# Kernel optimization log

Hardware: AMD Instinct MI355X
Metric: run time of the kernel (lower is better)

The kernel has to match this reference:

```python
import jax, jax.numpy as jnp
import numpy as np

RES = 32            # input grid resolution
OUT_RES = 64        # after subdivide
C = 128             # channels (== out_channels -> skip is identity)
G = 32              # group-norm groups
N = 8192            # active input voxels
EPS = 1e-5

# 8 child offsets for subdivide, 27 stencil offsets for 3x3x3 submanifold conv
_OFFS8 = np.stack(np.meshgrid([0, 1], [0, 1], [0, 1], indexing='ij'), -1).reshape(-1, 3).astype(np.int32)
_OFFS27 = np.stack(np.meshgrid([-1, 0, 1], [-1, 0, 1], [-1, 0, 1], indexing='ij'), -1).reshape(-1, 3).astype(np.int32)


def group_norm(x, gamma, beta, num_groups=G, eps=EPS):
    # sparse group norm over all active voxels of the (single) sample
    n, c = x.shape
    xg = x.reshape(n, num_groups, c // num_groups)
    mean = xg.mean(axis=(0, 2), keepdims=True)
    var = xg.var(axis=(0, 2), keepdims=True)
    xn = (xg - mean) * jax.lax.rsqrt(var + eps)
    return xn.reshape(n, c) * gamma + beta


def subdivide_coords(coords):
    offs = jnp.asarray(_OFFS8)
    return (coords[:, None, :] * 2 + offs[None, :, :]).reshape(-1, 3)  # [8N, 3]


def subm_conv3d(feats, coords, W, b, grid_res):
    # submanifold 3x3x3 sparse conv: outputs only at active sites
    n = feats.shape[0]
    grid = jnp.full((grid_res, grid_res, grid_res), -1, dtype=jnp.int32)
    grid = grid.at[coords[:, 0], coords[:, 1], coords[:, 2]].set(
        jnp.arange(n, dtype=jnp.int32))
    out = jnp.zeros((n, W.shape[-1]), dtype=feats.dtype)
    for k in range(27):  # fixed small stencil loop
        off = jnp.asarray(_OFFS27[k])
        nb = coords + off
        inb = jnp.all((nb >= 0) & (nb < grid_res), axis=1)
        nbc = jnp.clip(nb, 0, grid_res - 1)
        idx = grid[nbc[:, 0], nbc[:, 1], nbc[:, 2]]
        mask = inb & (idx >= 0)
        g = jnp.where(mask[:, None], feats[jnp.where(mask, idx, 0)], 0.0)
        out = out + g @ W[k]
    return out + b


def setup_inputs() -> dict:
    key = jax.random.key(0)
    ks = jax.random.split(key, 8)
    rng = np.random.default_rng(0)
    flat = rng.choice(RES ** 3, size=N, replace=False)
    coords = np.stack([flat // (RES * RES), (flat // RES) % RES, flat % RES],
                      axis=-1).astype(np.int32)
    feats = jax.random.normal(ks[0], (N, C), dtype=jnp.float32)
    gamma1 = 1.0 + 0.1 * jax.random.normal(ks[1], (C,), dtype=jnp.float32)
    beta1 = 0.1 * jax.random.normal(ks[2], (C,), dtype=jnp.float32)
    W1 = jax.random.normal(ks[3], (27, C, C), dtype=jnp.float32) * 0.05
    b1 = jax.random.normal(ks[4], (C,), dtype=jnp.float32) * 0.05
    gamma2 = 1.0 + 0.1 * jax.random.normal(ks[5], (C,), dtype=jnp.float32)
    beta2 = 0.1 * jax.random.normal(ks[6], (C,), dtype=jnp.float32)
    W2 = jax.random.normal(ks[7], (27, C, C), dtype=jnp.float32) * 0.05
    b2 = jax.random.normal(jax.random.fold_in(key, 99), (C,), dtype=jnp.float32) * 0.05
    return {"feats": feats, "gamma1": gamma1, "beta1": beta1, "W1": W1,
            "b1": b1, "gamma2": gamma2, "beta2": beta2, "W2": W2, "b2": b2,
            "coords": jnp.asarray(coords)}


def reference(feats, gamma1, beta1, W1, b1, gamma2, beta2, W2, b2, coords):
    # act_layers: GroupNorm + SiLU at input resolution
    h = jax.nn.silu(group_norm(feats, gamma1, beta1))
    # subdivide both branch and residual (8 children per voxel)
    new_coords = subdivide_coords(coords)          # [8N, 3] in OUT_RES grid
    h = jnp.repeat(h, 8, axis=0)
    x_sub = jnp.repeat(feats, 8, axis=0)
    # out_layers: conv3 -> GN -> SiLU -> conv3 (submanifold, same active set)
    h = subm_conv3d(h, new_coords, W1, b1, OUT_RES)
    h = jax.nn.silu(group_norm(h, gamma2, beta2))
    h = subm_conv3d(h, new_coords, W2, b2, OUT_RES)
    # skip_connection is Identity since out_channels == channels
    return h + x_sub
```

## Files before the change

### kernel.cpp

```cpp
#include <hip/hip_runtime.h>

#define NPAR   8192
#define NCH    65536
#define RES    32
#define EPS    1e-5f

typedef __attribute__((ext_vector_type(8))) short short8;
typedef __attribute__((ext_vector_type(4))) float floatx4;

__device__ __forceinline__ unsigned short f2bf(float f) {
    union { float f; unsigned u; } v; v.f = f;
    unsigned r = v.u + 0x7fffu + ((v.u >> 16) & 1u);
    return (unsigned short)(r >> 16);
}
__device__ __forceinline__ float bf2f(unsigned short b) {
    union { unsigned u; float f; } v; v.u = ((unsigned)b) << 16;
    return v.f;
}
__device__ __forceinline__ void glds16(const void* g, void* l) {
    __builtin_amdgcn_global_load_lds(
        (__attribute__((address_space(1))) const void*)g,
        (__attribute__((address_space(3))) void*)l, 16, 0, 0);
}
__device__ __forceinline__ int k27_of(int o, int s) {
    return (((o >> 2) & 1) + ((s >> 2) & 1)) * 9 +
           (((o >> 1) & 1) + ((s >> 1) & 1)) * 3 +
           ((o & 1) + (s & 1));
}
__device__ __forceinline__ void axis_dlist(int o, int s, int* d, int& n) {
    if (o == 0) { if (s == 0) { d[0] = -1; n = 1; } else { d[0] = 0; d[1] = 1; n = 2; } }
    else        { if (s == 0) { d[0] = -1; d[1] = 0; n = 2; } else { d[0] = 1; n = 1; } }
}

__global__ void k1_kernel(const int* __restrict__ coords, int* __restrict__ grid32,
                          const float* __restrict__ x, float* __restrict__ sum,
                          float* __restrict__ sq,
                          const float* __restrict__ W1, const float* __restrict__ W2,
                          unsigned short* __restrict__ Wc1f, unsigned short* __restrict__ Wp2) {
    int b = blockIdx.x;
    int t = threadIdx.x;
    if (b < 32) {
        int p = b * 256 + t;
        grid32[(coords[p*3] << 10) + (coords[p*3+1] << 5) + coords[p*3+2]] = p;
    } else if (b < 248) {
        int rem = (b - 32) * 256 + t;
        int lane = rem & 63;
        int ks   = (rem >> 6) & 3;
        int nb   = (rem >> 8) & 7;
        int tap  = rem >> 11;
        int n  = nb * 16 + (lane & 15);
        int k0 = ks * 32 + (lane >> 4) * 8;
        unsigned short v[8];
#pragma unroll
        for (int j = 0; j < 8; ++j) v[j] = f2bf(W2[tap * 16384 + (k0 + j) * 128 + n]);
        uint4 pk;
        pk.x = (unsigned)v[0] | ((unsigned)v[1] << 16);
        pk.y = (unsigned)v[2] | ((unsigned)v[3] << 16);
        pk.z = (unsigned)v[4] | ((unsigned)v[5] << 16);
        pk.w = (unsigned)v[6] | ((unsigned)v[7] << 16);
        *(uint4*)&Wp2[(long)rem * 8] = pk;
    } else if (b < 760) {
        int rem = (b - 248) * 256 + t;
        int lane  = rem & 63;
        int ks    = (rem >> 6) & 3;
        int nb    = (rem >> 8) & 7;
        int combo = rem >> 11;
        int o = combo >> 3, s = combo & 7;
        int n  = nb * 16 + (lane & 15);
        int k0 = ks * 32 + (lane >> 4) * 8;
        int d0[2], d1[2], d2[2], n0, n1, n2;
        axis_dlist((o >> 2) & 1, (s >> 2) & 1, d0, n0);
        axis_dlist((o >> 1) & 1, (s >> 1) & 1, d1, n1);
        axis_dlist(o & 1,        s & 1,        d2, n2);
        unsigned short v[8];
#pragma unroll
        for (int j = 0; j < 8; ++j) {
            float acc = 0.0f;
            for (int a = 0; a < n0; ++a)
                for (int bb = 0; bb < n1; ++bb)
                    for (int cc = 0; cc < n2; ++cc) {
                        int kk = (d0[a] + 1) * 9 + (d1[bb] + 1) * 3 + (d2[cc] + 1);
                        acc += W1[kk * 16384 + (k0 + j) * 128 + n];
                    }
            v[j] = f2bf(acc);
        }
        uint4 pk;
        pk.x = (unsigned)v[0] | ((unsigned)v[1] << 16);
        pk.y = (unsigned)v[2] | ((unsigned)v[3] << 16);
        pk.z = (unsigned)v[4] | ((unsigned)v[5] << 16);
        pk.w = (unsigned)v[6] | ((unsigned)v[7] << 16);
        *(uint4*)&Wc1f[(long)rem * 8] = pk;
    } else {
        __shared__ float s_sum[32], s_sq[32];
        if (t < 32) { s_sum[t] = 0.0f; s_sq[t] = 0.0f; }
        __syncthreads();
        const float4* x4 = (const float4*)x;
        int total = NPAR * 32;
        int idx0 = (b - 760) * 256 + t;
        int g = idx0 & 31;
        float ls = 0.0f, lq = 0.0f;
        for (int idx = idx0; idx < total; idx += 256 * 256) {
            float4 v = x4[idx];
            ls += v.x + v.y + v.z + v.w;
            lq += v.x * v.x + v.y * v.y + v.z * v.z + v.w * v.w;
        }
        atomicAdd(&s_sum[g], ls);
        atomicAdd(&s_sq[g], lq);
        __syncthreads();
        if (t < 32) { atomicAdd(&sum[t], s_sum[t]); atomicAdd(&sq[t], s_sq[t]); }
    }
}

__global__ void k2_kernel(const int* __restrict__ coords, const int* __restrict__ grid32,
                          int* __restrict__ idx_tab, int* __restrict__ pidx27,
                          const float* __restrict__ x, const float* __restrict__ sum,
                          const float* __restrict__ sq, const float* __restrict__ gamma,
                          const float* __restrict__ beta, unsigned short* __restrict__ y) {
    int b = blockIdx.x;
    if (b < 32) {
        int p = b * 256 + threadIdx.x;
        int cx = coords[p*3], cy = coords[p*3+1], cz = coords[p*3+2];
        int r27[27];
#pragma unroll
        for (int k = 0; k < 27; ++k) {
            int nx = cx + k / 9 - 1, ny = cy + (k / 3) % 3 - 1, nz = cz + k % 3 - 1;
            int r = -1;
            if ((unsigned)nx < 32u && (unsigned)ny < 32u && (unsigned)nz < 32u) {
                int g = grid32[(nx << 10) + (ny << 5) + nz];
                if ((unsigned)g < (unsigned)NPAR) r = g;
            }
            r27[k] = r;
            pidx27[k * NPAR + p] = r;
        }
#pragma unroll
        for (int k = 0; k < 27; ++k) {
            const int dx = k / 9 - 1, dy = (k / 3) % 3 - 1, dz = k % 3 - 1;
            int v[8];
#pragma unroll
            for (int o = 0; o < 8; ++o) {
                const int ex = ((o >> 2) & 1) + dx;
                const int ey = ((o >> 1) & 1) + dy;
                const int ez = (o & 1) + dz;
                const int ptap = ((ex >> 1) + 1) * 9 + ((ey >> 1) + 1) * 3 + ((ez >> 1) + 1);
                const int slot = ((ex & 1) << 2) + ((ey & 1) << 1) + (ez & 1);
                int r = r27[ptap];
                v[o] = (r >= 0) ? slot * NPAR + r : -1;
            }
            int4* dst = (int4*)&idx_tab[k * NCH + p * 8];
            dst[0] = make_int4(v[0], v[1], v[2], v[3]);
            dst[1] = make_int4(v[4], v[5], v[6], v[7]);
        }
    } else {
        const float4* x4 = (const float4*)x;
        uint2* y2 = (uint2*)y;
        const float4* g4 = (const float4*)gamma;
        const float4* b4 = (const float4*)beta;
        float cnt = (float)NPAR * 4.0f;
        int total = NPAR * 32;
        for (int idx = (b - 32) * 256 + threadIdx.x; idx < total; idx += 256 * 256) {
            int c4 = idx & 31;
            float mean = sum[c4] / cnt;
            float var = sq[c4] / cnt - mean * mean;
            float rstd = rsqrtf(var + EPS);
            float4 v = x4[idx];
            float4 gm = g4[c4];
            float4 bt = b4[c4];
            float a[4] = {v.x, v.y, v.z, v.w};
            float gg[4] = {gm.x, gm.y, gm.z, gm.w};
            float bb[4] = {bt.x, bt.y, bt.z, bt.w};
            unsigned short o[4];
#pragma unroll
            for (int i = 0; i < 4; ++i) {
                float tv = (a[i] - mean) * rstd * gg[i] + bb[i];
                o[i] = f2bf(tv / (1.0f + __expf(-tv)));
            }
            uint2 pk;
            pk.x = (unsigned)o[0] | ((unsigned)o[1] << 16);
            pk.y = (unsigned)o[2] | ((unsigned)o[3] << 16);
            y2[idx] = pk;
        }
    }
}

__global__ void gn_apply_bf16_kernel(unsigned short* __restrict__ x,
                                     const float* __restrict__ sum, const float* __restrict__ sq,
                                     const float* __restrict__ gamma, const float* __restrict__ beta,
                                     int nrows) {
    uint2* x2 = (uint2*)x;
    const float4* g4 = (const float4*)gamma;
    const float4* b4 = (const float4*)beta;
    float cnt = (float)nrows * 4.0f;
    int total = nrows * 32;
    for (int idx = blockIdx.x * blockDim.x + threadIdx.x; idx < total;
         idx += gridDim.x * blockDim.x) {
        int c4 = idx & 31;
        float mean = sum[c4] / cnt;
        float var = sq[c4] / cnt - mean * mean;
        float rstd = rsqrtf(var + EPS);
        uint2 pk = x2[idx];
        float a[4] = {bf2f((unsigned short)(pk.x & 0xffff)), bf2f((unsigned short)(pk.x >> 16)),
                      bf2f((unsigned short)(pk.y & 0xffff)), bf2f((unsigned short)(pk.y >> 16))};
        float4 gm = g4[c4];
        float4 bt = b4[c4];
        float gg[4] = {gm.x, gm.y, gm.z, gm.w};
        float bb[4] = {bt.x, bt.y, bt.z, bt.w};
        unsigned short o[4];
#pragma unroll
        for (int i = 0; i < 4; ++i) {
            float tv = (a[i] - mean) * rstd * gg[i] + bb[i];
            o[i] = f2bf(tv / (1.0f + __expf(-tv)));
        }
        pk.x = (unsigned)o[0] | ((unsigned)o[1] << 16);
        pk.y = (unsigned)o[2] | ((unsigned)o[3] << 16);
        x2[idx] = pk;
    }
}

__device__ __forceinline__ void mfma_phase(
    const unsigned short* __restrict__ Abuf, short8 (&bfr)[2][4],
    floatx4 (&acc)[8][2], int aswz) {
#pragma unroll
    for (int ks = 0; ks < 4; ++ks) {
        short8 afr[8];
#pragma unroll
        for (int mt = 0; mt < 8; ++mt)
            afr[mt] = *(const short8*)&Abuf[(mt << 11) + (ks << 9) + aswz];
#pragma unroll
        for (int mt = 0; mt < 8; ++mt)
#pragma unroll
            for (int nt = 0; nt < 2; ++nt)
                acc[mt][nt] = __builtin_amdgcn_mfma_f32_16x16x32_bf16(
                    afr[mt], bfr[nt][ks], acc[mt][nt], 0, 0, 0);
    }
}
__device__ __forceinline__ void loadB(const unsigned short* __restrict__ Wtap,
                                      short8 (&bfr)[2][4], int wn, int lane) {
#pragma unroll
    for (int nt = 0; nt < 2; ++nt)
#pragma unroll
        for (int ks = 0; ks < 4; ++ks)
            bfr[nt][ks] = *(const short8*)&Wtap[(((wn * 2 + nt) << 2) + ks) * 512 + (lane << 3)];
}
__device__ __forceinline__ void stageA(const unsigned short* __restrict__ Ag,
                                       int iv0, int iv1, const unsigned short* zsrc,
                                       unsigned short* __restrict__ buf,
                                       int base0, int base1, int cchOff) {
    const unsigned short* g0 = (iv0 >= 0) ? Ag + (long)iv0 * 128 : zsrc;
    const unsigned short* g1 = (iv1 >= 0) ? Ag + (long)iv1 * 128 : zsrc;
#pragma unroll
    for (int i = 0; i < 4; ++i) glds16(g0 + i * 32 + cchOff, &buf[base0 + i * 512]);
#pragma unroll
    for (int i = 0; i < 4; ++i) glds16(g1 + i * 32 + cchOff, &buf[base1 + i * 512]);
}

__global__ void __launch_bounds__(256, 2) conv1_fold_kernel(
    const unsigned short* __restrict__ Ag, const unsigned short* __restrict__ Wc1f,
    const float* __restrict__ bias, const int* __restrict__ pidx27,
    unsigned short* __restrict__ outp, const float* __restrict__ zpage,
    float* __restrict__ gsum, float* __restrict__ gsq) {
    __shared__ unsigned short A_lds[2][16384];

    int t = threadIdx.x;
    int o  = blockIdx.x & 7;
    int P0 = (blockIdx.x >> 3) << 7;
    const unsigned short* Wb = Wc1f + ((long)o << 17);
    int wv = t >> 6, lane = t & 63, quad = lane >> 4, l16 = lane & 15;
    int wn = wv;
    int r16 = lane >> 2, cch = lane & 3;
    int c0 = wv * 2, c1 = wv * 2 + 1;
    int row0 = ((c0 >> 2) << 6) + ((c0 & 3) << 4) + r16;
    int row1 = ((c1 >> 2) << 6) + ((c1 & 3) << 4) + r16;
    int base0 = ((c0 >> 2) << 13) + ((c0 & 3) << 11);
    int base1 = ((c1 >> 2) << 13) + ((c1 & 3) << 11);
    int cchOff = (cch ^ ((r16 >> 1) & 3)) << 3;
    int aswz = (l16 << 5) + ((quad ^ ((l16 >> 1) & 3)) << 3);
    const unsigned short* zsrc = (const unsigned short*)zpage;

    floatx4 acc[8][2];
#pragma unroll
    for (int mt = 0; mt < 8; ++mt)
#pragma unroll
        for (int nt = 0; nt < 2; ++nt)
            acc[mt][nt] = (floatx4){0.f, 0.f, 0.f, 0.f};
    short8 bA[2][4], bB[2][4];

    stageA(Ag, pidx27[k27_of(o, 0) * NPAR + P0 + row0],
               pidx27[k27_of(o, 0) * NPAR + P0 + row1], zsrc, A_lds[0], base0, base1, cchOff);
    loadB(Wb, bA, wn, lane);
    int nv0 = pidx27[k27_of(o, 1) * NPAR + P0 + row0];
    int nv1 = pidx27[k27_of(o, 1) * NPAR + P0 + row1];
    __syncthreads();

#pragma unroll 1
    for (int s = 0; s < 8; s += 2) {
        stageA(Ag, nv0, nv1, zsrc, A_lds[1], base0, base1, cchOff);
        loadB(Wb + ((long)(s + 1) << 14), bB, wn, lane);
        if (s + 2 < 8) {
            nv0 = pidx27[k27_of(o, s + 2) * NPAR + P0 + row0];
            nv1 = pidx27[k27_of(o, s + 2) * NPAR + P0 + row1];
        }
        mfma_phase(A_lds[0], bA, acc, aswz);
        __syncthreads();
        if (s + 2 < 8) {
            stageA(Ag, nv0, nv1, zsrc, A_lds[0], base0, base1, cchOff);
            loadB(Wb + ((long)(s + 2) << 14), bA, wn, lane);
            if (s + 3 < 8) {
                nv0 = pidx27[k27_of(o, s + 3) * NPAR + P0 + row0];
                nv1 = pidx27[k27_of(o, s + 3) * NPAR + P0 + row1];
            }
        }
        mfma_phase(A_lds[1], bB, acc, aswz);
        __syncthreads();
    }

    unsigned short* lds_s = (unsigned short*)A_lds;
    float* sred = (float*)(&A_lds[1][0]);
    float s_[2] = {0.f, 0.f}, q_[2] = {0.f, 0.f};
#pragma unroll
    for (int nt = 0; nt < 2; ++nt) {
        int col = wn * 32 + nt * 16 + l16;
        float bv = bias[col];
#pragma unroll
        for (int mt = 0; mt < 8; ++mt) {
#pragma unroll
            for (int r = 0; r < 4; ++r) {
                int row = mt * 16 + quad * 4 + r;
                float v = acc[mt][nt][r] + bv;
                unsigned short u = f2bf(v);
                lds_s[row * 128 + (col ^ (quad << 4))] = u;
                float vr = bf2f(u);
                s_[nt] += vr;
                q_[nt] += vr * vr;
            }
        }
    }
    if (t < 64) sred[t] = 0.0f;
    __syncthreads();
#pragma unroll
    for (int it = 0; it < 8; ++it) {
        int f = it * 256 + t;
        int row = f >> 4, c = (f & 15) * 8;
        int sw = ((row >> 2) & 3) << 4;
        uint4 v = *(const uint4*)&lds_s[row * 128 + (c ^ sw)];
        *(uint4*)&outp[((long)o * NPAR + P0 + row) * 128 + c] = v;
    }
#pragma unroll
    for (int nt = 0; nt < 2; ++nt) {
        int g = (wn * 32 + nt * 16 + l16) >> 2;
        atomicAdd(&sred[g], s_[nt]);
        atomicAdd(&sred[32 + g], q_[nt]);
    }
    __syncthreads();
    if (t < 32) { atomicAdd(&gsum[t], sred[t]); atomicAdd(&gsq[t], sred[32 + t]); }
}

__global__ void __launch_bounds__(256, 2) conv2_kernel(
    const unsigned short* __restrict__ Ag, const unsigned short* __restrict__ Wp,
    const float* __restrict__ bias, const int* __restrict__ idx_tab,
    const float* __restrict__ resid, float* __restrict__ outp,
    const float* __restrict__ zpage) {
    __shared__ unsigned short A_lds[2][16384];

    int t = threadIdx.x;
    int R0 = blockIdx.x * 128;
    int wv = t >> 6, lane = t & 63, quad = lane >> 4, l16 = lane & 15;
    int wn = wv;
    int r16 = lane >> 2, cch = lane & 3;
    int c0 = wv * 2, c1 = wv * 2 + 1;
    int row0 = ((c0 >> 2) << 6) + ((c0 & 3) << 4) + r16;
    int row1 = ((c1 >> 2) << 6) + ((c1 & 3) << 4) + r16;
    int base0 = ((c0 >> 2) << 13) + ((c0 & 3) << 11);
    int base1 = ((c1 >> 2) << 13) + ((c1 & 3) << 11);
    int cchOff = (cch ^ ((r16 >> 1) & 3)) << 3;
    int aswz = (l16 << 5) + ((quad ^ ((l16 >> 1) & 3)) << 3);
    const unsigned short* zsrc = (const unsigned short*)zpage;

    floatx4 acc[8][2];
#pragma unroll
    for (int mt = 0; mt < 8; ++mt)
#pragma unroll
        for (int nt = 0; nt < 2; ++nt)
            acc[mt][nt] = (floatx4){0.f, 0.f, 0.f, 0.f};
    short8 bA[2][4], bB[2][4];

    stageA(Ag, idx_tab[R0 + row0], idx_tab[R0 + row1], zsrc, A_lds[0], base0, base1, cchOff);
    loadB(Wp, bA, wn, lane);
    int nv0 = idx_tab[NCH + R0 + row0], nv1 = idx_tab[NCH + R0 + row1];
    __syncthreads();

#pragma unroll 1
    for (int k = 0; k < 27; k += 2) {
        if (k + 1 < 27) {
            stageA(Ag, nv0, nv1, zsrc, A_lds[1], base0, base1, cchOff);
            loadB(Wp + ((long)(k + 1) << 14), bB, wn, lane);
            if (k + 2 < 27) {
                nv0 = idx_tab[(k + 2) * NCH + R0 + row0];
                nv1 = idx_tab[(k + 2) * NCH + R0 + row1];
            }
        }
        mfma_phase(A_lds[0], bA, acc, aswz);
        __syncthreads();
        if (k + 1 < 27) {
            if (k + 2 < 27) {
                stageA(Ag, nv0, nv1, zsrc, A_lds[0], base0, base1, cchOff);
                loadB(Wp + ((long)(k + 2) << 14), bA, wn, lane);
                if (k + 3 < 27) {
                    nv0 = idx_tab[(k + 3) * NCH + R0 + row0];
                    nv1 = idx_tab[(k + 3) * NCH + R0 + row1];
                }
            }
            mfma_phase(A_lds[1], bB, acc, aswz);
            __syncthreads();
        }
    }

    float* lds_f = (float*)A_lds;
#pragma unroll
    for (int nt = 0; nt < 2; ++nt) {
        int col = wn * 32 + nt * 16 + l16;
        float bv = bias[col];
#pragma unroll
        for (int mt = 0; mt < 8; ++mt) {
#pragma unroll
            for (int r = 0; r < 4; ++r) {
                int row = mt * 16 + quad * 4 + r;
                long R = (long)R0 + row;
                float v = acc[mt][nt][r] + bv + resid[(R >> 3) * 128 + col];
                lds_f[row * 128 + (col ^ (quad << 4))] = v;
            }
        }
    }
    __syncthreads();
#pragma unroll
    for (int it = 0; it < 16; ++it) {
        int f = it * 256 + t;
        int row = f >> 5, c = (f & 31) * 4;
        int sw = ((row >> 2) & 3) << 4;
        float4 v = *(const float4*)&lds_f[row * 128 + (c ^ sw)];
        *(float4*)&outp[((long)R0 + row) * 128 + c] = v;
    }
}

extern "C" void kernel_launch(void* const* d_in, const int* in_sizes, int n_in,
                              void* d_out, int out_size, void* d_ws, size_t ws_size,
                              hipStream_t stream) {
    const float* feats  = (const float*)d_in[0];
    const float* gamma1 = (const float*)d_in[1];
    const float* beta1  = (const float*)d_in[2];
    const float* W1     = (const float*)d_in[3];
    const float* b1     = (const float*)d_in[4];
    const float* gamma2 = (const float*)d_in[5];
    const float* beta2  = (const float*)d_in[6];
    const float* W2     = (const float*)d_in[7];
    const float* b2     = (const float*)d_in[8];
    const int*   coords = (const int*)d_in[9];
    float* out = (float*)d_out;

    char* ws = (char*)d_ws;
    unsigned short* h0b  = (unsigned short*)(ws);
    unsigned short* h1b  = (unsigned short*)(ws + (2u << 20));
    unsigned short* Wc1f = (unsigned short*)(ws + (18u << 20));
    unsigned short* Wp2  = (unsigned short*)(ws + (20u << 20));
    int*   grid32        = (int*)  (ws + (21u << 20));
    float* stats         = (float*)(ws + (21u << 20) + 131072);
    float* zpage         = (float*)(ws + (21u << 20) + 131072 + 512);
    int*   idx_tab       = (int*)  (ws + (22u << 20));
    int*   pidx27        = (int*)  (ws + (30u << 20));

    hipMemsetAsync(stats, 0, 1024, stream);

    k1_kernel<<<1016, 256, 0, stream>>>(coords, grid32, feats, stats + 0, stats + 32,
                                        W1, W2, Wc1f, Wp2);
    k2_kernel<<<288, 256, 0, stream>>>(coords, grid32, idx_tab, pidx27,
                                       feats, stats + 0, stats + 32, gamma1, beta1, h0b);

    conv1_fold_kernel<<<8 * (NPAR / 128), 256, 0, stream>>>(h0b, Wc1f, b1, pidx27,
                                                            h1b, zpage,
                                                            stats + 64, stats + 96);

    gn_apply_bf16_kernel<<<1024, 256, 0, stream>>>(h1b, stats + 64, stats + 96, gamma2, beta2, NCH);

    conv2_kernel<<<NCH / 128, 256, 0, stream>>>(h1b, Wp2, b2, idx_tab,
                                                feats, out, zpage);
}
```

Before: 202.4 us.

## Fuse all five stages into one cooperative persistent kernel with grid syncs

Replaces the five separate launches (setup/weights, index tables + GN1, conv1, GN2 apply, conv2) with a single cooperative kernel of 512 blocks that separates the phases with grid-wide barriers. The goal is to remove per-launch overhead and the gaps between kernels. The old launch sequence remains as a fallback if the cooperative launch fails. The trade-off is that the grid is fixed at 512 blocks (two per CU), which must all be co-resident, and grid syncs stall every block until the slowest one finishes each phase.

```diff
diff --git a/kernel.cpp b/kernel.cpp
--- a/kernel.cpp
+++ b/kernel.cpp
@@ -1,9 +1,13 @@
 #include <hip/hip_runtime.h>
+#include <hip/hip_cooperative_groups.h>
+
+namespace cg = cooperative_groups;
 
 #define NPAR   8192
 #define NCH    65536
 #define RES    32
 #define EPS    1e-5f
+#define GRIDSZ (512 * 256)
 
 typedef __attribute__((ext_vector_type(8))) short short8;
 typedef __attribute__((ext_vector_type(4))) float floatx4;
@@ -30,6 +34,408 @@
 __device__ __forceinline__ void axis_dlist(int o, int s, int* d, int& n) {
     if (o == 0) { if (s == 0) { d[0] = -1; n = 1; } else { d[0] = 0; d[1] = 1; n = 2; } }
     else        { if (s == 0) { d[0] = -1; d[1] = 0; n = 2; } else { d[0] = 1; n = 1; } }
+}
+
+__device__ __forceinline__ void mfma_phase(
+    const unsigned short* __restrict__ Abuf, short8 (&bfr)[2][4],
+    floatx4 (&acc)[8][2], int aswz) {
+#pragma unroll
+    for (int ks = 0; ks < 4; ++ks) {
+        short8 afr[8];
+#pragma unroll
+        for (int mt = 0; mt < 8; ++mt)
+            afr[mt] = *(const short8*)&Abuf[(mt << 11) + (ks << 9) + aswz];
+#pragma unroll
+        for (int mt = 0; mt < 8; ++mt)
+#pragma unroll
+            for (int nt = 0; nt < 2; ++nt)
+                acc[mt][nt] = __builtin_amdgcn_mfma_f32_16x16x32_bf16(
+                    afr[mt], bfr[nt][ks], acc[mt][nt], 0, 0, 0);
+    }
+}
+__device__ __forceinline__ void loadB(const unsigned short* __restrict__ Wtap,
+                                      short8 (&bfr)[2][4], int wn, int lane) {
+#pragma unroll
+    for (int nt = 0; nt < 2; ++nt)
+#pragma unroll
+        for (int ks = 0; ks < 4; ++ks)
+            bfr[nt][ks] = *(const short8*)&Wtap[(((wn * 2 + nt) << 2) + ks) * 512 + (lane << 3)];
+}
+__device__ __forceinline__ void stageA(const unsigned short* __restrict__ Ag,
+                                       int iv0, int iv1, const unsigned short* zsrc,
+                                       unsigned short* __restrict__ buf,
+                                       int base0, int base1, int cchOff) {
+    const unsigned short* g0 = (iv0 >= 0) ? Ag + (long)iv0 * 128 : zsrc;
+    const unsigned short* g1 = (iv1 >= 0) ? Ag + (long)iv1 * 128 : zsrc;
+#pragma unroll
+    for (int i = 0; i < 4; ++i) glds16(g0 + i * 32 + cchOff, &buf[base0 + i * 512]);
+#pragma unroll
+    for (int i = 0; i < 4; ++i) glds16(g1 + i * 32 + cchOff, &buf[base1 + i * 512]);
+}
+
+__global__ void __launch_bounds__(256, 2) fused_kernel(
+    const int* __restrict__ coords, int* __restrict__ grid32,
+    const float* __restrict__ feats, float* __restrict__ stats,
+    const float* __restrict__ W1, const float* __restrict__ W2,
+    unsigned short* __restrict__ Wc1f, unsigned short* __restrict__ Wp2,
+    int* __restrict__ idx_tab, int* __restrict__ pidx27,
+    const float* __restrict__ gamma1, const float* __restrict__ beta1,
+    unsigned short* __restrict__ h0b,
+    const float* __restrict__ bias1, unsigned short* __restrict__ h1b,
+    const float* __restrict__ gamma2, const float* __restrict__ beta2,
+    const float* __restrict__ bias2, float* __restrict__ out,
+    const float* __restrict__ zpage) {
+    cg::grid_group gg = cg::this_grid();
+    __shared__ unsigned short A_lds[2][16384];
+
+    const int t = threadIdx.x, b = blockIdx.x;
+    const int tid = b * 256 + t;
+    float* sum1 = stats;      float* sq1 = stats + 32;
+    float* sum2 = stats + 64; float* sq2 = stats + 96;
+
+    if (tid < NPAR) {
+        grid32[(coords[tid*3] << 10) + (coords[tid*3+1] << 5) + coords[tid*3+2]] = tid;
+    }
+    if (tid < 55296) {
+        int lane = tid & 63;
+        int ks   = (tid >> 6) & 3;
+        int nb   = (tid >> 8) & 7;
+        int tap  = tid >> 11;
+        int n  = nb * 16 + (lane & 15);
+        int k0 = ks * 32 + (lane >> 4) * 8;
+        unsigned short v[8];
+#pragma unroll
+        for (int j = 0; j < 8; ++j) v[j] = f2bf(W2[tap * 16384 + (k0 + j) * 128 + n]);
+        uint4 pk;
+        pk.x = (unsigned)v[0] | ((unsigned)v[1] << 16);
+        pk.y = (unsigned)v[2] | ((unsigned)v[3] << 16);
+        pk.z = (unsigned)v[4] | ((unsigned)v[5] << 16);
+        pk.w = (unsigned)v[6] | ((unsigned)v[7] << 16);
+        *(uint4*)&Wp2[(long)tid * 8] = pk;
+    }
+    {
+        int rem = tid;
+        int lane  = rem & 63;
+        int ks    = (rem >> 6) & 3;
+        int nb    = (rem >> 8) & 7;
+        int combo = rem >> 11;
+        int o = combo >> 3, s = combo & 7;
+        int n  = nb * 16 + (lane & 15);
+        int k0 = ks * 32 + (lane >> 4) * 8;
+        int d0[2], d1[2], d2[2], n0, n1, n2;
+        axis_dlist((o >> 2) & 1, (s >> 2) & 1, d0, n0);
+        axis_dlist((o >> 1) & 1, (s >> 1) & 1, d1, n1);
+        axis_dlist(o & 1,        s & 1,        d2, n2);
+        unsigned short v[8];
+#pragma unroll
+        for (int j = 0; j < 8; ++j) {
+            float acc = 0.0f;
+            for (int a = 0; a < n0; ++a)
+                for (int bb = 0; bb < n1; ++bb)
+                    for (int cc = 0; cc < n2; ++cc) {
+                        int kk = (d0[a] + 1) * 9 + (d1[bb] + 1) * 3 + (d2[cc] + 1);
+                        acc += W1[kk * 16384 + (k0 + j) * 128 + n];
+                    }
+            v[j] = f2bf(acc);
+        }
+        uint4 pk;
+        pk.x = (unsigned)v[0] | ((unsigned)v[1] << 16);
+        pk.y = (unsigned)v[2] | ((unsigned)v[3] << 16);
+        pk.z = (unsigned)v[4] | ((unsigned)v[5] << 16);
+        pk.w = (unsigned)v[6] | ((unsigned)v[7] << 16);
+        *(uint4*)&Wc1f[(long)rem * 8] = pk;
+    }
+    {
+        float* s_sum = (float*)(&A_lds[0][0]);
+        float* s_sq  = s_sum + 32;
+        if (t < 32) { s_sum[t] = 0.0f; s_sq[t] = 0.0f; }
+        __syncthreads();
+        const float4* x4 = (const float4*)feats;
+        int g = tid & 31;
+        float ls = 0.0f, lq = 0.0f;
+        for (int idx = tid; idx < NPAR * 32; idx += GRIDSZ) {
+            float4 v = x4[idx];
+            ls += v.x + v.y + v.z + v.w;
+            lq += v.x * v.x + v.y * v.y + v.z * v.z + v.w * v.w;
+        }
+        atomicAdd(&s_sum[g], ls);
+        atomicAdd(&s_sq[g], lq);
+        __syncthreads();
+        if (t < 32) { atomicAdd(&sum1[t], s_sum[t]); atomicAdd(&sq1[t], s_sq[t]); }
+        __syncthreads();
+    }
+    gg.sync();
+
+    if (tid < NPAR) {
+        int p = tid;
+        int cx = coords[p*3], cy = coords[p*3+1], cz = coords[p*3+2];
+        int r27[27];
+#pragma unroll
+        for (int k = 0; k < 27; ++k) {
+            int nx = cx + k / 9 - 1, ny = cy + (k / 3) % 3 - 1, nz = cz + k % 3 - 1;
+            int r = -1;
+            if ((unsigned)nx < 32u && (unsigned)ny < 32u && (unsigned)nz < 32u) {
+                int g = grid32[(nx << 10) + (ny << 5) + nz];
+                if ((unsigned)g < (unsigned)NPAR) r = g;
+            }
+            r27[k] = r;
+            pidx27[k * NPAR + p] = r;
+        }
+#pragma unroll
+        for (int k = 0; k < 27; ++k) {
+            const int dx = k / 9 - 1, dy = (k / 3) % 3 - 1, dz = k % 3 - 1;
+            int v[8];
+#pragma unroll
+            for (int o = 0; o < 8; ++o) {
+                const int ex = ((o >> 2) & 1) + dx;
+                const int ey = ((o >> 1) & 1) + dy;
+                const int ez = (o & 1) + dz;
+                const int ptap = ((ex >> 1) + 1) * 9 + ((ey >> 1) + 1) * 3 + ((ez >> 1) + 1);
+                const int slot = ((ex & 1) << 2) + ((ey & 1) << 1) + (ez & 1);
+                int r = r27[ptap];
+                v[o] = (r >= 0) ? slot * NPAR + r : -1;
+            }
+            int4* dst = (int4*)&idx_tab[k * NCH + p * 8];
+            dst[0] = make_int4(v[0], v[1], v[2], v[3]);
+            dst[1] = make_int4(v[4], v[5], v[6], v[7]);
+        }
+    }
+    {
+        const float4* x4 = (const float4*)feats;
+        uint2* y2 = (uint2*)h0b;
+        const float4* g4 = (const float4*)gamma1;
+        const float4* b4 = (const float4*)beta1;
+        float cnt = (float)NPAR * 4.0f;
+        for (int idx = tid; idx < NPAR * 32; idx += GRIDSZ) {
+            int c4 = idx & 31;
+            float mean = sum1[c4] / cnt;
+            float var = sq1[c4] / cnt - mean * mean;
+            float rstd = rsqrtf(var + EPS);
+            float4 v = x4[idx];
+            float4 gm = g4[c4];
+            float4 bt = b4[c4];
+            float a[4] = {v.x, v.y, v.z, v.w};
+            float gq[4] = {gm.x, gm.y, gm.z, gm.w};
+            float bq[4] = {bt.x, bt.y, bt.z, bt.w};
+            unsigned short o[4];
+#pragma unroll
+            for (int i = 0; i < 4; ++i) {
+                float tv = (a[i] - mean) * rstd * gq[i] + bq[i];
+                o[i] = f2bf(tv / (1.0f + __expf(-tv)));
+            }
+            uint2 pk;
+            pk.x = (unsigned)o[0] | ((unsigned)o[1] << 16);
+            pk.y = (unsigned)o[2] | ((unsigned)o[3] << 16);
+            y2[idx] = pk;
+        }
+    }
+    gg.sync();
+
+    {
+        int o  = b & 7;
+        int P0 = (b >> 3) << 7;
+        const unsigned short* Wb = Wc1f + ((long)o << 17);
+        int wv = t >> 6, lane = t & 63, quad = lane >> 4, l16 = lane & 15;
+        int wn = wv;
+        int r16 = lane >> 2, cch = lane & 3;
+        int c0 = wv * 2, c1 = wv * 2 + 1;
+        int row0 = ((c0 >> 2) << 6) + ((c0 & 3) << 4) + r16;
+        int row1 = ((c1 >> 2) << 6) + ((c1 & 3) << 4) + r16;
+        int base0 = ((c0 >> 2) << 13) + ((c0 & 3) << 11);
+        int base1 = ((c1 >> 2) << 13) + ((c1 & 3) << 11);
+        int cchOff = (cch ^ ((r16 >> 1) & 3)) << 3;
+        int aswz = (l16 << 5) + ((quad ^ ((l16 >> 1) & 3)) << 3);
+        const unsigned short* zsrc = (const unsigned short*)zpage;
+
+        floatx4 acc[8][2];
+#pragma unroll
+        for (int mt = 0; mt < 8; ++mt)
+#pragma unroll
+            for (int nt = 0; nt < 2; ++nt)
+                acc[mt][nt] = (floatx4){0.f, 0.f, 0.f, 0.f};
+        short8 bA[2][4], bB[2][4];
+
+        stageA(h0b, pidx27[k27_of(o, 0) * NPAR + P0 + row0],
+                    pidx27[k27_of(o, 0) * NPAR + P0 + row1], zsrc, A_lds[0], base0, base1, cchOff);
+        loadB(Wb, bA, wn, lane);
+        int nv0 = pidx27[k27_of(o, 1) * NPAR + P0 + row0];
+        int nv1 = pidx27[k27_of(o, 1) * NPAR + P0 + row1];
+        __syncthreads();
+
+#pragma unroll 1
+        for (int s = 0; s < 8; s += 2) {
+            stageA(h0b, nv0, nv1, zsrc, A_lds[1], base0, base1, cchOff);
+            loadB(Wb + ((long)(s + 1) << 14), bB, wn, lane);
+            if (s + 2 < 8) {
+                nv0 = pidx27[k27_of(o, s + 2) * NPAR + P0 + row0];
+                nv1 = pidx27[k27_of(o, s + 2) * NPAR + P0 + row1];
+            }
+            mfma_phase(A_lds[0], bA, acc, aswz);
+            __syncthreads();
+            if (s + 2 < 8) {
+                stageA(h0b, nv0, nv1, zsrc, A_lds[0], base0, base1, cchOff);
+                loadB(Wb + ((long)(s + 2) << 14), bA, wn, lane);
+                if (s + 3 < 8) {
+                    nv0 = pidx27[k27_of(o, s + 3) * NPAR + P0 + row0];
+                    nv1 = pidx27[k27_of(o, s + 3) * NPAR + P0 + row1];
+                }
+            }
+            mfma_phase(A_lds[1], bB, acc, aswz);
+            __syncthreads();
+        }
+
+        unsigned short* lds_s = (unsigned short*)A_lds;
+        float* sred = (float*)(&A_lds[1][0]);
+        float s_[2] = {0.f, 0.f}, q_[2] = {0.f, 0.f};
+#pragma unroll
+        for (int nt = 0; nt < 2; ++nt) {
+            int col = wn * 32 + nt * 16 + l16;
+            float bv = bias1[col];
+#pragma unroll
+            for (int mt = 0; mt < 8; ++mt) {
+#pragma unroll
+                for (int r = 0; r < 4; ++r) {
+                    int row = mt * 16 + quad * 4 + r;
+                    float v = acc[mt][nt][r] + bv;
+                    unsigned short u = f2bf(v);
+                    lds_s[row * 128 + (col ^ (quad << 4))] = u;
+                    float vr = bf2f(u);
+                    s_[nt] += vr;
+                    q_[nt] += vr * vr;
+                }
+            }
+        }
+        if (t < 64) sred[t] = 0.0f;
+        __syncthreads();
+#pragma unroll
+        for (int it = 0; it < 8; ++it) {
+            int f = it * 256 + t;
+            int row = f >> 4, c = (f & 15) * 8;
+            int sw = ((row >> 2) & 3) << 4;
+            uint4 v = *(const uint4*)&lds_s[row * 128 + (c ^ sw)];
+            *(uint4*)&h1b[((long)o * NPAR + P0 + row) * 128 + c] = v;
+        }
+#pragma unroll
+        for (int nt = 0; nt < 2; ++nt) {
+            int g = (wn * 32 + nt * 16 + l16) >> 2;
+            atomicAdd(&sred[g], s_[nt]);
+            atomicAdd(&sred[32 + g], q_[nt]);
+        }
+        __syncthreads();
+        if (t < 32) { atomicAdd(&sum2[t], sred[t]); atomicAdd(&sq2[t], sred[32 + t]); }
+        __syncthreads();
+    }
+    gg.sync();
+
+    {
+        uint2* x2 = (uint2*)h1b;
+        const float4* g4 = (const float4*)gamma2;
+        const float4* b4 = (const float4*)beta2;
+        float cnt = (float)NCH * 4.0f;
+        for (int idx = tid; idx < NCH * 32; idx += GRIDSZ) {
+            int c4 = idx & 31;
+            float mean = sum2[c4] / cnt;
+            float var = sq2[c4] / cnt - mean * mean;
+            float rstd = rsqrtf(var + EPS);
+            uint2 pk = x2[idx];
+            float a[4] = {bf2f((unsigned short)(pk.x & 0xffff)), bf2f((unsigned short)(pk.x >> 16)),
+                          bf2f((unsigned short)(pk.y & 0xffff)), bf2f((unsigned short)(pk.y >> 16))};
+            float4 gm = g4[c4];
+            float4 bt = b4[c4];
+            float gq[4] = {gm.x, gm.y, gm.z, gm.w};
+            float bq[4] = {bt.x, bt.y, bt.z, bt.w};
+            unsigned short o[4];
+#pragma unroll
+            for (int i = 0; i < 4; ++i) {
+                float tv = (a[i] - mean) * rstd * gq[i] + bq[i];
+                o[i] = f2bf(tv / (1.0f + __expf(-tv)));
+            }
+            pk.x = (unsigned)o[0] | ((unsigned)o[1] << 16);
+            pk.y = (unsigned)o[2] | ((unsigned)o[3] << 16);
+            x2[idx] = pk;
+        }
+    }
+    gg.sync();
+
+    {
+        int R0 = b * 128;
+        int wv = t >> 6, lane = t & 63, quad = lane >> 4, l16 = lane & 15;
+        int wn = wv;
+        int r16 = lane >> 2, cch = lane & 3;
+        int c0 = wv * 2, c1 = wv * 2 + 1;
+        int row0 = ((c0 >> 2) << 6) + ((c0 & 3) << 4) + r16;
+        int row1 = ((c1 >> 2) << 6) + ((c1 & 3) << 4) + r16;
+        int base0 = ((c0 >> 2) << 13) + ((c0 & 3) << 11);
+        int base1 = ((c1 >> 2) << 13) + ((c1 & 3) << 11);
+        int cchOff = (cch ^ ((r16 >> 1) & 3)) << 3;
+        int aswz = (l16 << 5) + ((quad ^ ((l16 >> 1) & 3)) << 3);
+        const unsigned short* zsrc = (const unsigned short*)zpage;
+
+        floatx4 acc[8][2];
+#pragma unroll
+        for (int mt = 0; mt < 8; ++mt)
+#pragma unroll
+            for (int nt = 0; nt < 2; ++nt)
+                acc[mt][nt] = (floatx4){0.f, 0.f, 0.f, 0.f};
+        short8 bA[2][4], bB[2][4];
+
+        stageA(h1b, idx_tab[R0 + row0], idx_tab[R0 + row1], zsrc, A_lds[0], base0, base1, cchOff);
+        loadB(Wp2, bA, wn, lane);
+        int nv0 = idx_tab[NCH + R0 + row0], nv1 = idx_tab[NCH + R0 + row1];
+        __syncthreads();
+
+#pragma unroll 1
+        for (int k = 0; k < 27; k += 2) {
+            if (k + 1 < 27) {
+                stageA(h1b, nv0, nv1, zsrc, A_lds[1], base0, base1, cchOff);
+                loadB(Wp2 + ((long)(k + 1) << 14), bB, wn, lane);
+                if (k + 2 < 27) {
+                    nv0 = idx_tab[(k + 2) * NCH + R0 + row0];
+                    nv1 = idx_tab[(k + 2) * NCH + R0 + row1];
+                }
+            }
+            mfma_phase(A_lds[0], bA, acc, aswz);
+            __syncthreads();
+            if (k + 1 < 27) {
+                if (k + 2 < 27) {
+                    stageA(h1b, nv0, nv1, zsrc, A_lds[0], base0, base1, cchOff);
+                    loadB(Wp2 + ((long)(k + 2) << 14), bA, wn, lane);
+                    if (k + 3 < 27) {
+                        nv0 = idx_tab[(k + 3) * NCH + R0 + row0];
+                        nv1 = idx_tab[(k + 3) * NCH + R0 + row1];
+                    }
+                }
+                mfma_phase(A_lds[1], bB, acc, aswz);
+                __syncthreads();
+            }
+        }
+
+        float* lds_f = (float*)A_lds;
+#pragma unroll
+        for (int nt = 0; nt < 2; ++nt) {
+            int col = wn * 32 + nt * 16 + l16;
+            float bv = bias2[col];
+#pragma unroll
+            for (int mt = 0; mt < 8; ++mt) {
+#pragma unroll
+                for (int r = 0; r < 4; ++r) {
+                    int row = mt * 16 + quad * 4 + r;
+                    long R = (long)R0 + row;
+                    float v = acc[mt][nt][r] + bv + feats[(R >> 3) * 128 + col];
+                    lds_f[row * 128 + (col ^ (quad << 4))] = v;
+                }
+            }
+        }
+        __syncthreads();
+#pragma unroll
+        for (int it = 0; it < 16; ++it) {
+            int f = it * 256 + t;
+            int row = f >> 5, c = (f & 31) * 4;
+            int sw = ((row >> 2) & 3) << 4;
+            float4 v = *(const float4*)&lds_f[row * 128 + (c ^ sw)];
+            *(float4*)&out[((long)R0 + row) * 128 + c] = v;
+        }
+    }
 }
 
 __global__ void k1_kernel(const int* __restrict__ coords, int* __restrict__ grid32,
@@ -216,43 +622,6 @@
     }
 }
 
-__device__ __forceinline__ void mfma_phase(
-    const unsigned short* __restrict__ Abuf, short8 (&bfr)[2][4],
-    floatx4 (&acc)[8][2], int aswz) {
-#pragma unroll
-    for (int ks = 0; ks < 4; ++ks) {
-        short8 afr[8];
-#pragma unroll
-        for (int mt = 0; mt < 8; ++mt)
-            afr[mt] = *(const short8*)&Abuf[(mt << 11) + (ks << 9) + aswz];
-#pragma unroll
-        for (int mt = 0; mt < 8; ++mt)
-#pragma unroll
-            for (int nt = 0; nt < 2; ++nt)
-                acc[mt][nt] = __builtin_amdgcn_mfma_f32_16x16x32_bf16(
-                    afr[mt], bfr[nt][ks], acc[mt][nt], 0, 0, 0);
-    }
-}
-__device__ __forceinline__ void loadB(const unsigned short* __restrict__ Wtap,
-                                      short8 (&bfr)[2][4], int wn, int lane) {
-#pragma unroll
-    for (int nt = 0; nt < 2; ++nt)
-#pragma unroll
-        for (int ks = 0; ks < 4; ++ks)
-            bfr[nt][ks] = *(const short8*)&Wtap[(((wn * 2 + nt) << 2) + ks) * 512 + (lane << 3)];
-}
-__device__ __forceinline__ void stageA(const unsigned short* __restrict__ Ag,
-                                       int iv0, int iv1, const unsigned short* zsrc,
-                                       unsigned short* __restrict__ buf,
-                                       int base0, int base1, int cchOff) {
-    const unsigned short* g0 = (iv0 >= 0) ? Ag + (long)iv0 * 128 : zsrc;
-    const unsigned short* g1 = (iv1 >= 0) ? Ag + (long)iv1 * 128 : zsrc;
-#pragma unroll
-    for (int i = 0; i < 4; ++i) glds16(g0 + i * 32 + cchOff, &buf[base0 + i * 512]);
-#pragma unroll
-    for (int i = 0; i < 4; ++i) glds16(g1 + i * 32 + cchOff, &buf[base1 + i * 512]);
-}
-
 __global__ void __launch_bounds__(256, 2) conv1_fold_kernel(
     const unsigned short* __restrict__ Ag, const unsigned short* __restrict__ Wc1f,
     const float* __restrict__ bias, const int* __restrict__ pidx27,
@@ -469,17 +838,28 @@
 
     hipMemsetAsync(stats, 0, 1024, stream);
 
+    void* args[] = {
+        (void*)&coords, (void*)&grid32, (void*)&feats, (void*)&stats,
+        (void*)&W1, (void*)&W2, (void*)&Wc1f, (void*)&Wp2,
+        (void*)&idx_tab, (void*)&pidx27,
+        (void*)&gamma1, (void*)&beta1, (void*)&h0b,
+        (void*)&b1, (void*)&h1b,
+        (void*)&gamma2, (void*)&beta2,
+        (void*)&b2, (void*)&out, (void*)&zpage
+    };
+    hipError_t e = hipLaunchCooperativeKernel(
+        reinterpret_cast<const void*>(fused_kernel),
+        dim3(512), dim3(256), args, 0, stream);
+    if (e == hipSuccess) return;
+
     k1_kernel<<<1016, 256, 0, stream>>>(coords, grid32, feats, stats + 0, stats + 32,
                                         W1, W2, Wc1f, Wp2);
     k2_kernel<<<288, 256, 0, stream>>>(coords, grid32, idx_tab, pidx27,
                                        feats, stats + 0, stats + 32, gamma1, beta1, h0b);
-
     conv1_fold_kernel<<<8 * (NPAR / 128), 256, 0, stream>>>(h0b, Wc1f, b1, pidx27,
                                                             h1b, zpage,
                                                             stats + 64, stats + 96);
-
     gn_apply_bf16_kernel<<<1024, 256, 0, stream>>>(h1b, stats + 64, stats + 96, gamma2, beta2, NCH);
-
     conv2_kernel<<<NCH / 128, 256, 0, stream>>>(h1b, Wp2, b2, idx_tab,
                                                 feats, out, zpage);
 }
```

Result: slower. 435.2 us (+115.0%).
